# Kernel optimization log

Measured on AMD Instinct MI355X. Metric: run time of the kernel, lower is better.

The kernel has to match this reference:

```python
import jax, jax.numpy as jnp
import numpy as np

DIM = 1024
HEADS = 16
HEAD_DIM = DIM // HEADS
B, S, L0, L1 = 2, 2048, 2048, 2048


def setup_inputs() -> dict:
    key = jax.random.key(0)
    ks = jax.random.split(key, 10)
    sc = DIM ** -0.5
    return {
        "query": jax.random.normal(ks[0], (B, S, DIM), jnp.float32),
        "l0_keys": jax.random.normal(ks[1], (B, L0, DIM), jnp.float32),
        "l0_values": jax.random.normal(ks[2], (B, L0, DIM), jnp.float32),
        "l1_keys": jax.random.normal(ks[3], (B, L1, DIM), jnp.float32),
        "l1_values": jax.random.normal(ks[4], (B, L1, DIM), jnp.float32),
        "l0_mask": jax.random.randint(ks[5], (S, L0), 0, 2, jnp.int32),
        "Wq": jax.random.normal(ks[6], (DIM, DIM), jnp.float32) * sc,
        "bq": jnp.zeros((DIM,), jnp.float32),
        "Wo": jax.random.normal(ks[7], (DIM, DIM), jnp.float32) * sc,
        "bo": jnp.zeros((DIM,), jnp.float32),
        "gate": jnp.asarray(0.0, jnp.float32),
    }


def reference(query, l0_keys, l0_values, l1_keys, l1_values, l0_mask, Wq, bq, Wo, bo, gate):
    b, s, d = query.shape
    h, hd = HEADS, HEAD_DIM
    scale = hd ** -0.5
    # q: [B,H,S,hd]
    q = (query @ Wq.T + bq).reshape(b, s, h, hd).transpose(0, 2, 1, 3)

    def attend(keys, values, mask):
        L = keys.shape[1]
        k = keys.reshape(b, L, h, hd)
        v = values.reshape(b, L, h, hd)
        scores = jnp.einsum("bhsd,blhd->bhsl", q, k) * scale
        if mask is not None:
            scores = jnp.where(mask[None, None] == 0, -jnp.inf, scores)
        w = jax.nn.softmax(scores, axis=-1)  # [B,H,S,L]
        out = jnp.einsum("bhsl,blhd->bshd", w, v)  # [B,S,H,hd]
        return out, w.mean(axis=1)

    out0, a0 = attend(l0_keys, l0_values, l0_mask)
    out1, a1 = attend(l1_keys, l1_values, None)
    g = jax.nn.sigmoid(gate)
    out = (g * out0 + (1.0 - g) * out1).reshape(b, s, d)
    out = out @ Wo.T + bo
    return out, a0, a1
```

## Files before the change

kernel.cpp:

```cpp
#include <hip/hip_runtime.h>

#define DIM   1024
#define HEADS 16
#define HD    64
#define BB    2
#define SS    2048
#define LLL   2048
#define LOG2E 1.4426950408889634f

typedef __bf16 bf16x8 __attribute__((ext_vector_type(8)));
typedef __bf16 bf16x4v __attribute__((ext_vector_type(4)));
typedef float  f32x4  __attribute__((ext_vector_type(4)));
typedef short  s16x4  __attribute__((ext_vector_type(4)));
typedef short  s16x8  __attribute__((ext_vector_type(8)));
typedef unsigned short u16;

static __device__ __forceinline__ u16 f2b(float x) {
  unsigned u = __float_as_uint(x);
  u += 0x7fffu + ((u >> 16) & 1u);
  return (u16)(u >> 16);
}
static __device__ __forceinline__ float b2f(u16 u) {
  return __uint_as_float(((unsigned)u) << 16);
}
static __device__ __forceinline__ f32x4 mfma32(bf16x8 a, bf16x8 b, f32x4 c) {
  return __builtin_amdgcn_mfma_f32_16x16x32_bf16(a, b, c, 0, 0, 0);
}
static __device__ __forceinline__ f32x4 mfma16(s16x4 a, s16x4 b, f32x4 c) {
#if __has_builtin(__builtin_amdgcn_mfma_f32_16x16x16bf16_1k)
  return __builtin_amdgcn_mfma_f32_16x16x16bf16_1k(a, b, c, 0, 0, 0);
#else
  asm volatile("v_mfma_f32_16x16x16_bf16 %0, %1, %2, %0" : "+v"(c) : "v"(a), "v"(b));
  return c;
#endif
}

static __device__ __forceinline__ void gload_lds16(const void* g, void* lds_uniform_base) {
#if __has_builtin(__builtin_amdgcn_global_load_lds)
  __builtin_amdgcn_global_load_lds(
      (const __attribute__((address_space(1))) unsigned int*)g,
      (__attribute__((address_space(3))) unsigned int*)lds_uniform_base, 16, 0, 0);
#else
  const int l = threadIdx.x & 63;
  ((uint4*)lds_uniform_base)[l] = ((const uint4*)g)[0];
#endif
}

__global__ void cvt_f32_bf16(const float* __restrict__ src, u16* __restrict__ dst, int n4) {
  int i = blockIdx.x * blockDim.x + threadIdx.x;
  if (i >= n4) return;
  float4 f = ((const float4*)src)[i];
  ushort4 o;
  o.x = f2b(f.x); o.y = f2b(f.y); o.z = f2b(f.z); o.w = f2b(f.w);
  ((ushort4*)dst)[i] = o;
}

__global__ void mask_pack(const int* __restrict__ mask, unsigned* __restrict__ mbits) {
  int i = blockIdx.x * blockDim.x + threadIdx.x;
  const int* src = mask + (size_t)i * 32;
  unsigned bm = 0;
#pragma unroll
  for (int j = 0; j < 8; ++j) {
    int4 m = ((const int4*)src)[j];
    bm |= (m.x != 0 ? 1u : 0u) << (j * 4 + 0);
    bm |= (m.y != 0 ? 1u : 0u) << (j * 4 + 1);
    bm |= (m.z != 0 ? 1u : 0u) << (j * 4 + 2);
    bm |= (m.w != 0 ? 1u : 0u) << (j * 4 + 3);
  }
  mbits[i] = bm;
}

__global__ __launch_bounds__(256) void pack_k(const float* __restrict__ k0,
                                              const float* __restrict__ k1,
                                              u16* __restrict__ Kfrag) {
  const float SCK = 0.125f * LOG2E;
  const int w = threadIdx.x >> 6, l = threadIdx.x & 63, g = l >> 4, li = l & 15;
  const int lt = blockIdx.x * 4 + w, h = blockIdx.y, z = blockIdx.z;
  const int lay = z >> 1, b = z & 1;
  const float* src = (lay ? k1 : k0) + (size_t)b * LLL * DIM;
  u16* dst = Kfrag + ((((size_t)z * HEADS + h) * 32 + lt) * 8) * 512;
#pragma unroll
  for (int c = 0; c < 8; ++c) {
    int mt = c >> 1, kk = c & 1;
    const float* p = &src[(size_t)(lt * 64 + mt * 16 + li) * DIM + h * 64 + kk * 32 + g * 8];
    float4 f0 = *(const float4*)p;
    float4 f1 = *(const float4*)(p + 4);
    u16 u[8] = {f2b(f0.x * SCK), f2b(f0.y * SCK), f2b(f0.z * SCK), f2b(f0.w * SCK),
                f2b(f1.x * SCK), f2b(f1.y * SCK), f2b(f1.z * SCK), f2b(f1.w * SCK)};
    *(uint4*)&dst[c * 512 + l * 8] = *(uint4*)u;
  }
}

__global__ __launch_bounds__(256) void pack_v(const float* __restrict__ v0,
                                              const float* __restrict__ v1,
                                              u16* __restrict__ Vfrag) {
  __shared__ u16 T[64][72];
  const int lt = blockIdx.x, h = blockIdx.y, z = blockIdx.z;
  const int lay = z >> 1, b = z & 1;
  const float* v = (lay ? v1 : v0) + (size_t)b * LLL * DIM;
  const int t = threadIdx.x;
  {
    int r = t >> 2, c16 = (t & 3) * 16;
    const float* src = &v[(size_t)(lt * 64 + r) * DIM + h * 64 + c16];
#pragma unroll
    for (int i = 0; i < 4; ++i) {
      float4 f = *(const float4*)&src[i * 4];
      T[r][c16 + i * 4 + 0] = f2b(f.x);
      T[r][c16 + i * 4 + 1] = f2b(f.y);
      T[r][c16 + i * 4 + 2] = f2b(f.z);
      T[r][c16 + i * 4 + 3] = f2b(f.w);
    }
  }
  __syncthreads();
  u16* dst = Vfrag + ((((size_t)z * HEADS + h) * 32 + lt) * 8) * 512;
  {
    int lane = t & 63, g = lane >> 4, li = lane & 15;
#pragma unroll
    for (int cc = 0; cc < 2; ++cc) {
      int c = (t >> 6) + cc * 4;
      int mt = c >> 1, p = c & 1;
      u16 u[8];
#pragma unroll
      for (int j = 0; j < 4; ++j) u[j] = T[mt * 16 + 4 * g + j][p * 32 + li];
#pragma unroll
      for (int j = 0; j < 4; ++j) u[4 + j] = T[mt * 16 + 4 * g + j][p * 32 + 16 + li];
      *(uint4*)&dst[c * 512 + lane * 8] = *(uint4*)u;
    }
  }
}

template<int MODE>
__global__ __launch_bounds__(256) void gemm_nt(const u16* __restrict__ A,
                                               const u16* __restrict__ Bt,
                                               const float* __restrict__ bias,
                                               void* __restrict__ Cv,
                                               int M, int N, int K) {
  __shared__ u16 As[128][64];
  __shared__ u16 Bs[64][64];
  const int t = threadIdx.x;
  const int w = t >> 6, l = t & 63, g = l >> 4, li = l & 15;
  const int m0 = blockIdx.y * 128, n0 = blockIdx.x * 64;
  const int slotL = w * 64 + l;
  const int rA = slotL >> 3, cA = ((slotL & 7) * 8) ^ ((rA & 7) * 8);
  f32x4 acc[2][4] = {};
  for (int kt = 0; kt < K; kt += 64) {
#pragma unroll
    for (int s = 0; s < 4; ++s) {
      int r = rA + s * 32;
      gload_lds16(&A[(size_t)(m0 + r) * K + kt + cA], &As[0][0] + (s * 256 + w * 64) * 8);
    }
#pragma unroll
    for (int s = 0; s < 2; ++s) {
      int r = rA + s * 32;
      gload_lds16(&Bt[(size_t)(n0 + r) * K + kt + cA], &Bs[0][0] + (s * 256 + w * 64) * 8);
    }
    __syncthreads();
#pragma unroll
    for (int kk = 0; kk < 2; ++kk) {
      bf16x8 a[2], bfr[4];
#pragma unroll
      for (int mi = 0; mi < 2; ++mi) {
        int ra = w * 32 + mi * 16 + li;
        a[mi] = *(const bf16x8*)&As[ra][(kk * 32 + g * 8) ^ ((ra & 7) << 3)];
      }
#pragma unroll
      for (int ni = 0; ni < 4; ++ni) {
        int rb = ni * 16 + li;
        bfr[ni] = *(const bf16x8*)&Bs[rb][(kk * 32 + g * 8) ^ ((rb & 7) << 3)];
      }
#pragma unroll
      for (int mi = 0; mi < 2; ++mi)
#pragma unroll
        for (int ni = 0; ni < 4; ++ni)
          acc[mi][ni] = mfma32(a[mi], bfr[ni], acc[mi][ni]);
    }
    __syncthreads();
  }
#pragma unroll
  for (int mi = 0; mi < 2; ++mi)
#pragma unroll
    for (int ni = 0; ni < 4; ++ni)
#pragma unroll
      for (int v = 0; v < 4; ++v) {
        int rr = m0 + w * 32 + mi * 16 + g * 4 + v;
        int cc = n0 + ni * 16 + li;
        float val = acc[mi][ni][v] + bias[cc];
        if (MODE == 1) {
          ((float*)Cv)[(size_t)rr * N + cc] = val;
        } else {
          int b = rr >> 11, q = rr & 2047;
          int qt = q >> 5, n = (q >> 4) & 1, liq = q & 15;
          int h = (cc >> 6) & 15, kk2 = (cc >> 5) & 1, gp = (cc >> 3) & 3, j = cc & 7;
          size_t base = ((((size_t)b * HEADS + h) * 64 + qt) * 4 + n * 2 + kk2) * 512;
          ((u16*)Cv)[base + (size_t)(gp * 16 + liq) * 8 + j] = f2b(val);
        }
      }
}

template<int MASKED>
static __device__ __forceinline__ void attn_pv_body(int z, int h, int qt, int w, int l,
                                                    const u16* __restrict__ Qfrag,
                                                    const u16* __restrict__ Kfrag,
                                                    const u16* __restrict__ Vfrag,
                                                    const unsigned* __restrict__ mbits,
                                                    u16* __restrict__ out01,
                                                    float* __restrict__ db,
                                                    u16* __restrict__ KV) {
  const int g = l >> 4, li = l & 15;
  const int b = z & 1;
  const u16* kfh = Kfrag + (size_t)(z * HEADS + h) * (32 * 8 * 512);
  const u16* vfh = Vfrag + (size_t)(z * HEADS + h) * (32 * 8 * 512);
  const u16* qfh = Qfrag + (((size_t)(b * HEADS + h) * 64 + qt) * 4) * 512;

  bf16x8 qf[2][2];
#pragma unroll
  for (int n = 0; n < 2; ++n)
#pragma unroll
    for (int kk = 0; kk < 2; ++kk)
      qf[n][kk] = *(const bf16x8*)&qfh[(n * 2 + kk) * 512 + l * 8];

  const unsigned* mrow0 = MASKED ? mbits + (size_t)(qt * 32 + li) * (LLL / 32) : nullptr;
  const unsigned* mrow1 = MASKED ? mrow0 + 16 * (LLL / 32) : nullptr;
  const int shb = 4 * g;
  const s16x4 ones = {(short)0x3F80, (short)0x3F80, (short)0x3F80, (short)0x3F80};

  auto stage = [&](int buf, int lt) {
    const u16* kfl = kfh + (size_t)lt * 4096;
    const u16* vfl = vfh + (size_t)lt * 4096;
#pragma unroll
    for (int i2 = 0; i2 < 2; ++i2) {
      int f = w * 2 + i2;
      const u16* gsrc = (f < 8 ? kfl + f * 512 : vfl + (f - 8) * 512) + l * 8;
      gload_lds16(gsrc, (char*)KV + buf * 16384 + f * 1024);
    }
  };

  f32x4 dacc[2] = {};
  f32x4 oacc[4][2] = {};

  stage(0, 0);
  __syncthreads();
  int cur = 0;
  for (int lt = 0; lt < 32; ++lt) {
    if (lt + 1 < 32) stage(cur ^ 1, lt + 1);
    unsigned mw[2][2];
    if (MASKED) {
      mw[0][0] = mrow0[lt * 2]; mw[0][1] = mrow0[lt * 2 + 1];
      mw[1][0] = mrow1[lt * 2]; mw[1][1] = mrow1[lt * 2 + 1];
    }
    const u16* Ks = KV + cur * 8192;
    const u16* Vs = Ks + 4096;
#pragma unroll
    for (int mt = 0; mt < 4; ++mt) {
      bf16x8 k0 = *(const bf16x8*)&Ks[(mt * 2 + 0) * 512 + l * 8];
      bf16x8 k1 = *(const bf16x8*)&Ks[(mt * 2 + 1) * 512 + l * 8];
      f32x4 s[2] = {};
      __builtin_amdgcn_s_setprio(1);
#pragma unroll
      for (int n = 0; n < 2; ++n) {
        s[n] = mfma32(k0, qf[n][0], s[n]);
        s[n] = mfma32(k1, qf[n][1], s[n]);
      }
      __builtin_amdgcn_s_setprio(0);
      s16x4 wpk[2];
#pragma unroll
      for (int n = 0; n < 2; ++n) {
        unsigned mm = MASKED ? (mw[n][mt >> 1] >> ((mt & 1) * 16 + shb)) : 0u;
        f32x4 ev;
#pragma unroll
        for (int v = 0; v < 4; ++v) {
          float e = __builtin_amdgcn_exp2f(s[n][v]);
          if (MASKED) {
            int spread = ((int)(mm << (31 - v))) >> 31;
            e = __uint_as_float(__float_as_uint(e) & (unsigned)spread);
          }
          ev[v] = e;
        }
        bf16x4v wb = __builtin_convertvector(ev, bf16x4v);
        wpk[n] = __builtin_bit_cast(s16x4, wb);
      }
      __builtin_amdgcn_s_setprio(1);
      dacc[0] = mfma16(ones, wpk[0], dacc[0]);
      dacc[1] = mfma16(ones, wpk[1], dacc[1]);
#pragma unroll
      for (int p = 0; p < 2; ++p) {
        s16x8 vf = *(const s16x8*)&Vs[(mt * 2 + p) * 512 + l * 8];
        s16x4 lo = __builtin_shufflevector(vf, vf, 0, 1, 2, 3);
        s16x4 hi = __builtin_shufflevector(vf, vf, 4, 5, 6, 7);
#pragma unroll
        for (int n = 0; n < 2; ++n) {
          oacc[2 * p + 0][n] = mfma16(lo, wpk[n], oacc[2 * p + 0][n]);
          oacc[2 * p + 1][n] = mfma16(hi, wpk[n], oacc[2 * p + 1][n]);
        }
      }
      __builtin_amdgcn_s_setprio(0);
    }
    __syncthreads();
    cur ^= 1;
  }
  float dinv[2];
  dinv[0] = 1.0f / dacc[0][0];
  dinv[1] = 1.0f / dacc[1][0];
  if (l < 16) {
    db[(size_t)(z * HEADS + h) * SS + qt * 32 + li]      = -__log2f(dacc[0][0]);
    db[(size_t)(z * HEADS + h) * SS + qt * 32 + 16 + li] = -__log2f(dacc[1][0]);
  }
  u16* ob = out01 + (size_t)z * SS * DIM;
#pragma unroll
  for (int dt = 0; dt < 4; ++dt)
#pragma unroll
    for (int n = 0; n < 2; ++n) {
      f32x4 o = oacc[dt][n] * dinv[n];
      ushort4 us;
      us.x = f2b(o[0]); us.y = f2b(o[1]); us.z = f2b(o[2]); us.w = f2b(o[3]);
      *(ushort4*)&ob[((size_t)(qt * 32 + n * 16 + li)) * DIM + h * HD + dt * 16 + 4 * g] = us;
    }
}

__global__ __launch_bounds__(512, 4) void attn_pv(const u16* __restrict__ Qfrag,
                                                  const u16* __restrict__ Kfrag,
                                                  const u16* __restrict__ Vfrag,
                                                  const unsigned* __restrict__ mbits,
                                                  u16* __restrict__ out01,
                                                  float* __restrict__ db) {
  __shared__ u16 KV[2][8192];
  const int flat = blockIdx.x;
  const int xcd = flat & 7, i = flat >> 3;
  const int k = i >> 3, qg = i & 7;
  const int zh = xcd + 8 * k;
  const int z = zh >> 4, h = zh & 15;
  const int w = threadIdx.x >> 6, l = threadIdx.x & 63;
  const int qt = qg * 8 + w;
  if (z < 2) attn_pv_body<1>(z, h, qt, w, l, Qfrag, Kfrag, Vfrag, mbits, out01, db, &KV[0][0]);
  else       attn_pv_body<0>(z, h, qt, w, l, Qfrag, Kfrag, Vfrag, mbits, out01, db, &KV[0][0]);
}

template<int MASKED>
static __device__ __forceinline__ void amean_body(int z, int qt, int lt, int w, int l,
                                                  const u16* __restrict__ Qfrag,
                                                  const u16* __restrict__ Kfrag,
                                                  const unsigned* __restrict__ mbits,
                                                  const float* __restrict__ db,
                                                  float* __restrict__ aout,
                                                  u16* __restrict__ KS) {
  const int g = l >> 4, li = l & 15;
  const int b = z & 1;

  unsigned mw[2][2];
  if (MASKED) {
    const unsigned* m0 = mbits + (size_t)(qt * 32 + li) * (LLL / 32) + lt * 2;
    const unsigned* m1 = m0 + 16 * (LLL / 32);
    mw[0][0] = m0[0]; mw[0][1] = m0[1];
    mw[1][0] = m1[0]; mw[1][1] = m1[1];
  }
  const u16* qf_base = Qfrag + (((size_t)(b * HEADS) * 64 + qt) * 4) * 512 + l * 8;
  const float* dbb = db + (size_t)(z * HEADS) * SS + qt * 32 + li;

  auto stageK = [&](int buf, int h) {
    const u16* kfh = Kfrag + ((((size_t)(z * HEADS + h)) * 32 + lt) * 8) * 512;
#pragma unroll
    for (int i2 = 0; i2 < 2; ++i2) {
      int f = w * 2 + i2;
      gload_lds16(kfh + f * 512 + l * 8, (char*)KS + buf * 8192 + f * 1024);
    }
  };

  f32x4 asum[4][2] = {};
  stageK(0, 0);
  __syncthreads();
#pragma unroll 2
  for (int h = 0; h < HEADS; ++h) {
    if (h + 1 < HEADS) stageK((h + 1) & 1, h + 1);
    float l2[2];
    l2[0] = dbb[(size_t)h * SS];
    l2[1] = dbb[(size_t)h * SS + 16];
    bf16x8 qf[2][2];
#pragma unroll
    for (int n = 0; n < 2; ++n)
#pragma unroll
      for (int kk = 0; kk < 2; ++kk)
        qf[n][kk] = *(const bf16x8*)&qf_base[(size_t)h * (64 * 4 * 512) + (n * 2 + kk) * 512];
    const u16* Ks = KS + (h & 1) * 4096;
#pragma unroll
    for (int mt = 0; mt < 4; ++mt) {
      bf16x8 k0 = *(const bf16x8*)&Ks[(mt * 2 + 0) * 512 + l * 8];
      bf16x8 k1 = *(const bf16x8*)&Ks[(mt * 2 + 1) * 512 + l * 8];
#pragma unroll
      for (int n = 0; n < 2; ++n) {
        f32x4 s = {};
        s = mfma32(k0, qf[n][0], s);
        s = mfma32(k1, qf[n][1], s);
        unsigned mm = MASKED ? (mw[n][mt >> 1] >> ((mt & 1) * 16 + 4 * g)) : 0u;
#pragma unroll
        for (int v = 0; v < 4; ++v) {
          float e = __builtin_amdgcn_exp2f(s[v] + l2[n]);
          if (MASKED) {
            int spread = ((int)(mm << (31 - v))) >> 31;
            e = __uint_as_float(__float_as_uint(e) & (unsigned)spread);
          }
          asum[mt][n][v] += e;
        }
      }
    }
    __syncthreads();
  }
  float* ab = aout + (size_t)z * SS * LLL;
#pragma unroll
  for (int mt = 0; mt < 4; ++mt)
#pragma unroll
    for (int n = 0; n < 2; ++n) {
      f32x4 o = asum[mt][n] * 0.0625f;
      f32x4* dst = (f32x4*)&ab[(size_t)(qt * 32 + n * 16 + li) * LLL + lt * 64 + mt * 16 + 4 * g];
      __builtin_nontemporal_store(o, dst);
    }
}

__global__ __launch_bounds__(256, 4) void amean(const u16* __restrict__ Qfrag,
                                                const u16* __restrict__ Kfrag,
                                                const unsigned* __restrict__ mbits,
                                                const float* __restrict__ db,
                                                float* __restrict__ aout) {
  __shared__ u16 KS[2][4096];
  const int flat = blockIdx.x;
  const int xcd = flat & 7, i = flat >> 3;
  const int k = i >> 4, qg = i & 15;
  const int zlt = xcd + 8 * k;
  const int z = zlt >> 5, lt = zlt & 31;
  const int w = threadIdx.x >> 6, l = threadIdx.x & 63;
  const int qt = qg * 4 + w;
  if (z < 2) amean_body<1>(z, qt, lt, w, l, Qfrag, Kfrag, mbits, db, aout, &KS[0][0]);
  else       amean_body<0>(z, qt, lt, w, l, Qfrag, Kfrag, mbits, db, aout, &KS[0][0]);
}

__global__ void merge_kernel(const u16* __restrict__ o01,
                             const float* __restrict__ gate,
                             u16* __restrict__ merged) {
  int i = blockIdx.x * blockDim.x + threadIdx.x;
  float gv = gate[0];
  float g = 1.0f / (1.0f + __builtin_amdgcn_exp2f(-gv * LOG2E));
  const size_t n = (size_t)BB * SS * DIM;
  ushort4 a = ((const ushort4*)o01)[i];
  ushort4 c = ((const ushort4*)(o01 + n))[i];
  ushort4 o;
  o.x = f2b(g * b2f(a.x) + (1.f - g) * b2f(c.x));
  o.y = f2b(g * b2f(a.y) + (1.f - g) * b2f(c.y));
  o.z = f2b(g * b2f(a.z) + (1.f - g) * b2f(c.z));
  o.w = f2b(g * b2f(a.w) + (1.f - g) * b2f(c.w));
  ((ushort4*)merged)[i] = o;
}

extern "C" void kernel_launch(void* const* d_in, const int* in_sizes, int n_in,
                              void* d_out, int out_size, void* d_ws, size_t ws_size,
                              hipStream_t stream) {
  const float* query = (const float*)d_in[0];
  const float* k0f   = (const float*)d_in[1];
  const float* v0f   = (const float*)d_in[2];
  const float* k1f   = (const float*)d_in[3];
  const float* v1f   = (const float*)d_in[4];
  const int*   mask  = (const int*)d_in[5];
  const float* Wqf   = (const float*)d_in[6];
  const float* bq    = (const float*)d_in[7];
  const float* Wof   = (const float*)d_in[8];
  const float* bo    = (const float*)d_in[9];
  const float* gate  = (const float*)d_in[10];
  float* out = (float*)d_out;

  const size_t nQ = (size_t)BB * SS * DIM;
  const size_t nW = (size_t)DIM * DIM;

  char* ws = (char*)d_ws;
  size_t off = 0;
  auto alloc = [&](size_t bytes) -> char* {
    char* p = ws + off;
    off += (bytes + 255) & ~(size_t)255;
    return p;
  };
  u16*      queryb  = (u16*)alloc(nQ * 2);
  u16*      wqb     = (u16*)alloc(nW * 2);
  u16*      wob     = (u16*)alloc(nW * 2);
  u16*      Qfrag   = (u16*)alloc(nQ * 2);
  u16*      Kfrag   = (u16*)alloc((size_t)2 * nQ * 2);
  u16*      Vfrag   = (u16*)alloc((size_t)2 * nQ * 2);
  unsigned* mbits   = (unsigned*)alloc((size_t)SS * (LLL / 32) * 4);
  float*    db      = (float*)alloc((size_t)4 * HEADS * SS * 4);
  u16*      out01   = (u16*)alloc((size_t)2 * nQ * 2);
  u16*      mergedb = queryb;

  auto cvt = [&](const float* s, u16* d, size_t n) {
    int n4 = (int)(n / 4);
    cvt_f32_bf16<<<dim3((n4 + 255) / 256), dim3(256), 0, stream>>>(s, d, n4);
  };
  cvt(query, queryb, nQ);
  cvt(Wqf, wqb, nW);
  cvt(Wof, wob, nW);

  mask_pack<<<dim3(SS * (LLL / 32) / 256), dim3(256), 0, stream>>>(mask, mbits);
  pack_k<<<dim3(LLL / 64 / 4, HEADS, 4), dim3(256), 0, stream>>>(k0f, k1f, Kfrag);
  pack_v<<<dim3(LLL / 64, HEADS, 4), dim3(256), 0, stream>>>(v0f, v1f, Vfrag);

  gemm_nt<2><<<dim3(DIM / 64, (BB * SS) / 128), dim3(256), 0, stream>>>(
      queryb, wqb, bq, (void*)Qfrag, BB * SS, DIM, DIM);

  attn_pv<<<dim3(512), dim3(512), 0, stream>>>(Qfrag, Kfrag, Vfrag, mbits, out01, db);

  amean<<<dim3(2048), dim3(256), 0, stream>>>(Qfrag, Kfrag, mbits, db, out + nQ);

  merge_kernel<<<dim3((int)(nQ / 4 / 256)), dim3(256), 0, stream>>>(out01, gate, mergedb);

  gemm_nt<1><<<dim3(DIM / 64, (BB * SS) / 128), dim3(256), 0, stream>>>(
      mergedb, wob, bo, (void*)out, BB * SS, DIM, DIM);
}
```

Baseline: 226.4 us.

## Double-buffer GEMM tiles, software-pipeline attention QK/PV, fuse bf16 converts

The GEMM kernel gets double-buffered LDS tiles so the next K-tile loads while MFMAs run on the current one, and one barrier per iteration is removed. In the attention inner loop, the QK score MFMAs for the next sub-tile are issued ahead of the softmax/PV work of the current one, so exp and MFMA work can interleave. The three f32→bf16 conversion launches are merged into a single kernel to cut launch overhead. This costs more LDS and registers, which may reduce occupancy.

```diff
diff --git a/kernel.cpp b/kernel.cpp
--- a/kernel.cpp
+++ b/kernel.cpp
@@ -46,13 +46,18 @@
 #endif
 }
 
-__global__ void cvt_f32_bf16(const float* __restrict__ src, u16* __restrict__ dst, int n4) {
+__global__ void cvt3(const float* __restrict__ a, const float* __restrict__ b,
+                     const float* __restrict__ c, u16* __restrict__ da,
+                     u16* __restrict__ db_, u16* __restrict__ dc, int na4, int nb4) {
   int i = blockIdx.x * blockDim.x + threadIdx.x;
-  if (i >= n4) return;
-  float4 f = ((const float4*)src)[i];
+  const float* s; u16* d; int j = i;
+  if (j < na4) { s = a; d = da; }
+  else if ((j -= na4) < nb4) { s = b; d = db_; }
+  else { j -= nb4; s = c; d = dc; }
+  float4 f = ((const float4*)s)[j];
   ushort4 o;
   o.x = f2b(f.x); o.y = f2b(f.y); o.z = f2b(f.z); o.w = f2b(f.w);
-  ((ushort4*)dst)[i] = o;
+  ((ushort4*)d)[j] = o;
 }
 
 __global__ void mask_pack(const int* __restrict__ mask, unsigned* __restrict__ mbits) {
@@ -135,38 +140,45 @@
                                                const float* __restrict__ bias,
                                                void* __restrict__ Cv,
                                                int M, int N, int K) {
-  __shared__ u16 As[128][64];
-  __shared__ u16 Bs[64][64];
+  __shared__ u16 As[2][128][64];
+  __shared__ u16 Bs[2][64][64];
   const int t = threadIdx.x;
   const int w = t >> 6, l = t & 63, g = l >> 4, li = l & 15;
   const int m0 = blockIdx.y * 128, n0 = blockIdx.x * 64;
   const int slotL = w * 64 + l;
   const int rA = slotL >> 3, cA = ((slotL & 7) * 8) ^ ((rA & 7) * 8);
-  f32x4 acc[2][4] = {};
-  for (int kt = 0; kt < K; kt += 64) {
+
+  auto stageAB = [&](int buf, int kt) {
 #pragma unroll
     for (int s = 0; s < 4; ++s) {
       int r = rA + s * 32;
-      gload_lds16(&A[(size_t)(m0 + r) * K + kt + cA], &As[0][0] + (s * 256 + w * 64) * 8);
+      gload_lds16(&A[(size_t)(m0 + r) * K + kt + cA], &As[buf][0][0] + (s * 256 + w * 64) * 8);
     }
 #pragma unroll
     for (int s = 0; s < 2; ++s) {
       int r = rA + s * 32;
-      gload_lds16(&Bt[(size_t)(n0 + r) * K + kt + cA], &Bs[0][0] + (s * 256 + w * 64) * 8);
-    }
-    __syncthreads();
+      gload_lds16(&Bt[(size_t)(n0 + r) * K + kt + cA], &Bs[buf][0][0] + (s * 256 + w * 64) * 8);
+    }
+  };
+
+  f32x4 acc[2][4] = {};
+  stageAB(0, 0);
+  __syncthreads();
+  int cur = 0;
+  for (int kt = 0; kt < K; kt += 64) {
+    if (kt + 64 < K) stageAB(cur ^ 1, kt + 64);
 #pragma unroll
     for (int kk = 0; kk < 2; ++kk) {
       bf16x8 a[2], bfr[4];
 #pragma unroll
       for (int mi = 0; mi < 2; ++mi) {
         int ra = w * 32 + mi * 16 + li;
-        a[mi] = *(const bf16x8*)&As[ra][(kk * 32 + g * 8) ^ ((ra & 7) << 3)];
+        a[mi] = *(const bf16x8*)&As[cur][ra][(kk * 32 + g * 8) ^ ((ra & 7) << 3)];
       }
 #pragma unroll
       for (int ni = 0; ni < 4; ++ni) {
         int rb = ni * 16 + li;
-        bfr[ni] = *(const bf16x8*)&Bs[rb][(kk * 32 + g * 8) ^ ((rb & 7) << 3)];
+        bfr[ni] = *(const bf16x8*)&Bs[cur][rb][(kk * 32 + g * 8) ^ ((rb & 7) << 3)];
       }
 #pragma unroll
       for (int mi = 0; mi < 2; ++mi)
@@ -175,6 +187,7 @@
           acc[mi][ni] = mfma32(a[mi], bfr[ni], acc[mi][ni]);
     }
     __syncthreads();
+    cur ^= 1;
   }
 #pragma unroll
   for (int mi = 0; mi < 2; ++mi)
@@ -250,18 +263,19 @@
     }
     const u16* Ks = KV + cur * 8192;
     const u16* Vs = Ks + 4096;
-#pragma unroll
-    for (int mt = 0; mt < 4; ++mt) {
+
+    auto qk = [&](f32x4 (&s)[2], int mt) {
       bf16x8 k0 = *(const bf16x8*)&Ks[(mt * 2 + 0) * 512 + l * 8];
       bf16x8 k1 = *(const bf16x8*)&Ks[(mt * 2 + 1) * 512 + l * 8];
-      f32x4 s[2] = {};
+      f32x4 zz = {};
       __builtin_amdgcn_s_setprio(1);
-#pragma unroll
-      for (int n = 0; n < 2; ++n) {
-        s[n] = mfma32(k0, qf[n][0], s[n]);
-        s[n] = mfma32(k1, qf[n][1], s[n]);
-      }
+      s[0] = mfma32(k0, qf[0][0], zz);
+      s[0] = mfma32(k1, qf[0][1], s[0]);
+      s[1] = mfma32(k0, qf[1][0], zz);
+      s[1] = mfma32(k1, qf[1][1], s[1]);
       __builtin_amdgcn_s_setprio(0);
+    };
+    auto sm_pv = [&](f32x4 (&s)[2], int mt) {
       s16x4 wpk[2];
 #pragma unroll
       for (int n = 0; n < 2; ++n) {
@@ -294,7 +308,14 @@
         }
       }
       __builtin_amdgcn_s_setprio(0);
-    }
+    };
+
+    f32x4 sA[2], sB[2];
+    qk(sA, 0);
+    qk(sB, 1); sm_pv(sA, 0);
+    qk(sA, 2); sm_pv(sB, 1);
+    qk(sB, 3); sm_pv(sA, 2);
+    sm_pv(sB, 3);
     __syncthreads();
     cur ^= 1;
   }
@@ -486,13 +507,11 @@
   u16*      out01   = (u16*)alloc((size_t)2 * nQ * 2);
   u16*      mergedb = queryb;
 
-  auto cvt = [&](const float* s, u16* d, size_t n) {
-    int n4 = (int)(n / 4);
-    cvt_f32_bf16<<<dim3((n4 + 255) / 256), dim3(256), 0, stream>>>(s, d, n4);
-  };
-  cvt(query, queryb, nQ);
-  cvt(Wqf, wqb, nW);
-  cvt(Wof, wob, nW);
+  {
+    int na4 = (int)(nQ / 4), nb4 = (int)(nW / 4);
+    int tot = na4 + 2 * nb4;
+    cvt3<<<dim3(tot / 256), dim3(256), 0, stream>>>(query, Wqf, Wof, queryb, wqb, wob, na4, nb4);
+  }
 
   mask_pack<<<dim3(SS * (LLL / 32) / 256), dim3(256), 0, stream>>>(mask, mbits);
   pack_k<<<dim3(LLL / 64 / 4, HEADS, 4), dim3(256), 0, stream>>>(k0f, k1f, Kfrag);
```

Measured after the change: 219.4 us. 1.03x faster.
